# Kernel optimization log

Hardware: AMD Instinct MI355X
Metric: run time of the kernel (lower is better)

The kernel has to match this reference:

```python
import jax, jax.numpy as jnp
import numpy as np

B, HEADS, SCALES, POINTS, HIDDEN = 1, 8, 4, 4, 192
HEAD_DIM = HIDDEN // HEADS
OFFSET_SCALE = 0.35
EPS = 1e-5


def conv1x1(x, W, b=None):
    # x: [B,C,D,H,W], W: [O,C]
    y = jnp.einsum('bcdhw,oc->bodhw', x, W)
    if b is not None:
        y = y + b[None, :, None, None, None]
    return y


def base_grid(D, H, W, dtype):
    z = jnp.linspace(-1.0, 1.0, D, dtype=dtype)
    y = jnp.linspace(-1.0, 1.0, H, dtype=dtype)
    x = jnp.linspace(-1.0, 1.0, W, dtype=dtype)
    zz, yy, xx = jnp.meshgrid(z, y, x, indexing='ij')
    return jnp.stack((xx, yy, zz), axis=-1)  # [D,H,W,3] (x,y,z order)


def trilinear_sample(val, grid):
    # val: [BH,C,Dv,Hv,Wv]; grid: [BH,N,3] normalized (x,y,z), align_corners=False, border padding
    BH, C, Dv, Hv, Wv = val.shape
    unnorm = lambda g, s: jnp.clip(((g + 1.0) * s - 1.0) * 0.5, 0.0, s - 1.0)
    ix = unnorm(grid[..., 0], Wv)
    iy = unnorm(grid[..., 1], Hv)
    iz = unnorm(grid[..., 2], Dv)
    x0f, y0f, z0f = jnp.floor(ix), jnp.floor(iy), jnp.floor(iz)
    wx, wy, wz = ix - x0f, iy - y0f, iz - z0f
    x0 = x0f.astype(jnp.int32); x1 = jnp.minimum(x0 + 1, Wv - 1)
    y0 = y0f.astype(jnp.int32); y1 = jnp.minimum(y0 + 1, Hv - 1)
    z0 = z0f.astype(jnp.int32); z1 = jnp.minimum(z0 + 1, Dv - 1)
    vflat = val.reshape(BH, C, Dv * Hv * Wv)
    gather = jax.vmap(lambda v, i: v[:, i])  # -> [BH,C,N]
    def corner(zi, yi, xi):
        return gather(vflat, (zi * Hv + yi) * Wv + xi)
    w = lambda a: a[:, None, :]  # broadcast weight over channel dim
    out = (corner(z0, y0, x0) * w((1 - wz) * (1 - wy) * (1 - wx))
           + corner(z0, y0, x1) * w((1 - wz) * (1 - wy) * wx)
           + corner(z0, y1, x0) * w((1 - wz) * wy * (1 - wx))
           + corner(z0, y1, x1) * w((1 - wz) * wy * wx)
           + corner(z1, y0, x0) * w(wz * (1 - wy) * (1 - wx))
           + corner(z1, y0, x1) * w(wz * (1 - wy) * wx)
           + corner(z1, y1, x0) * w(wz * wy * (1 - wx))
           + corner(z1, y1, x1) * w(wz * wy * wx))
    return out


def fsad_forward(query_feature, values, Wq, Wvs, Woff, boff, Wwt, bwt, Wout, gamma, beta):
    Bq, _, D, H, W = query_feature.shape
    N = D * H * W
    q = conv1x1(query_feature, Wq)
    off = conv1x1(q, Woff, boff).reshape(Bq, HEADS, SCALES, POINTS, 3, D, H, W)
    off = jnp.tanh(off) * OFFSET_SCALE
    aw = conv1x1(q, Wwt, bwt).reshape(Bq, HEADS, SCALES * POINTS, D, H, W)
    aw = jax.nn.softmax(aw, axis=2).reshape(Bq, HEADS, SCALES, POINTS, D, H, W)
    bg = base_grid(D, H, W, q.dtype)  # [D,H,W,3]
    acc = jnp.zeros((Bq, HEADS, HEAD_DIM, D, H, W), q.dtype)
    for s in range(SCALES):
        feat = values[s]
        val = conv1x1(feat, Wvs[s]).reshape(Bq * HEADS, HEAD_DIM, *feat.shape[2:])
        # off[:,:,s]: [B,Hh,P,3,D,H,W] -> grid [B,Hh,P,D,H,W,3]
        grid = bg[None, None, None] + jnp.moveaxis(off[:, :, s], 3, -1)
        grid = grid.reshape(Bq * HEADS, POINTS * N, 3)
        sampled = trilinear_sample(val, grid).reshape(Bq, HEADS, HEAD_DIM, POINTS, D, H, W)
        acc = acc + jnp.einsum('bhcpdyx,bhpdyx->bhcdyx', sampled, aw[:, :, s])
    out = conv1x1(acc.reshape(Bq, HIDDEN, D, H, W), Wout)
    # InstanceNorm3d(affine=True)
    mu = out.mean(axis=(2, 3, 4), keepdims=True)
    var = out.var(axis=(2, 3, 4), keepdims=True)
    out = (out - mu) * jax.lax.rsqrt(var + EPS)
    return out * gamma[None, :, None, None, None] + beta[None, :, None, None, None]


def setup_inputs() -> dict:
    key = jax.random.key(0)
    ks = jax.random.split(key, 16)
    value_channels = [32, 64, 128, 256]
    sizes = [64, 32, 16, 8]
    inp = {
        'query_feature': jax.random.normal(ks[0], (1, 128, 16, 16, 16), jnp.float32),
        'v0': jax.random.normal(ks[1], (1, 32, 64, 64, 64), jnp.float32),
        'v1': jax.random.normal(ks[2], (1, 64, 32, 32, 32), jnp.float32),
        'v2': jax.random.normal(ks[3], (1, 128, 16, 16, 16), jnp.float32),
        'v3': jax.random.normal(ks[4], (1, 256, 8, 8, 8), jnp.float32),
        'Wq': jax.random.normal(ks[5], (HIDDEN, 128), jnp.float32) * 0.05,
        'Wv0': jax.random.normal(ks[6], (HIDDEN, 32), jnp.float32) * 0.05,
        'Wv1': jax.random.normal(ks[7], (HIDDEN, 64), jnp.float32) * 0.05,
        'Wv2': jax.random.normal(ks[8], (HIDDEN, 128), jnp.float32) * 0.05,
        'Wv3': jax.random.normal(ks[9], (HIDDEN, 256), jnp.float32) * 0.05,
        'Woff': jax.random.normal(ks[10], (HEADS * SCALES * POINTS * 3, HIDDEN), jnp.float32) * 0.05,
        'boff': jnp.zeros((HEADS * SCALES * POINTS * 3,), jnp.float32),
        'Wwt': jax.random.normal(ks[11], (HEADS * SCALES * POINTS, HIDDEN), jnp.float32) * 0.05,
        'bwt': jnp.zeros((HEADS * SCALES * POINTS,), jnp.float32),
        'Wout': jax.random.normal(ks[12], (128, HIDDEN), jnp.float32) * 0.05,
        'gamma': jnp.ones((128,), jnp.float32),
        'beta': jnp.zeros((128,), jnp.float32),
    }
    return inp


def reference(query_feature, v0, v1, v2, v3, Wq, Wv0, Wv1, Wv2, Wv3, Woff, boff, Wwt, bwt, Wout, gamma, beta):
    return fsad_forward(query_feature, [v0, v1, v2, v3], Wq, [Wv0, Wv1, Wv2, Wv3], Woff, boff, Wwt, bwt, Wout, gamma, beta)
```

## Files before the change

### kernel.cpp

```cpp
#include <hip/hip_runtime.h>
#include <hip/hip_fp16.h>
#include <cmath>

#define N_Q 4096
#define HEADS 8
#define HEAD_DIM 24
#define HIDDEN 192

__device__ __forceinline__ float4 ld4(const float* p) { return *(const float4*)p; }

__device__ __forceinline__ void fma8h(float* u, float w, const __half* p) {
    uint4 raw = *(const uint4*)p;
    const __half2* h2 = reinterpret_cast<const __half2*>(&raw);
#pragma unroll
    for (int k = 0; k < 4; k++) {
        float2 f = __half22float2(h2[k]);
        u[2 * k]     = fmaf(w, f.x, u[2 * k]);
        u[2 * k + 1] = fmaf(w, f.y, u[2 * k + 1]);
    }
}

__device__ __forceinline__ void corner24(float* acc, float w, const __half* p) {
    fma8h(acc,      w, p);
    fma8h(acc + 8,  w, p + 8);
    fma8h(acc + 16, w, p + 16);
}


__device__ __forceinline__ void transpose_body(char* smem, const float* __restrict__ src,
                                               __half* __restrict__ dst, int bx, int tid)
{
    float (*lds)[33] = (float(*)[33])smem;
    const int Nv = 262144;
    int pos0 = bx * 256;
    for (int k = tid; k < 256 * 32; k += 256) {
        int c = k >> 8, p = k & 255;
        lds[p][c] = src[(size_t)c * Nv + pos0 + p];
    }
    __syncthreads();
    for (int k = tid; k < 256 * 32; k += 256) {
        int p = k >> 5, c = k & 31;
        dst[(size_t)(pos0 + p) * 32 + c] = __float2half(lds[p][c]);
    }
}

template<int C, int OG>
__device__ __forceinline__ void valconv_body(char* smem, const float* __restrict__ Wv,
                                             const float* __restrict__ v,
                                             __half* __restrict__ valT, int Nv,
                                             int bx, int by, int tid)
{
    float* Wl = (float*)smem;
    __half* outs = (__half*)(smem + OG * C * 4);
    int p0 = bx * 64;
    int og0 = by * OG;
    for (int k = tid; k < OG * C; k += 256) Wl[k] = Wv[(size_t)(og0 + k / C) * C + (k % C)];
    __syncthreads();

    int osub = tid >> 6;
    int lane = tid & 63;
    constexpr int PT = OG / 4;
    float acc[PT];
#pragma unroll
    for (int i = 0; i < PT; i++) acc[i] = 0.f;
#pragma unroll 2
    for (int c = 0; c < C; c++) {
        float vv = v[(size_t)c * Nv + p0 + lane];
#pragma unroll
        for (int i = 0; i < PT; i++)
            acc[i] = fmaf(Wl[(osub * PT + i) * C + c], vv, acc[i]);
    }
#pragma unroll
    for (int i = 0; i < PT; i++)
        outs[lane * OG + osub * PT + i] = __float2half(acc[i]);
    __syncthreads();

    unsigned int* dst = (unsigned int*)valT;
    const unsigned int* src = (const unsigned int*)outs;
    constexpr int UPP = OG / 2;
    for (int k = tid; k < 64 * UPP; k += 256) {
        int p = k / UPP, i = k % UPP;
        int hh = og0 / 24 + i / 12;
        int ii = i % 12;
        dst[((size_t)hh * Nv + p0 + p) * 12 + ii] = src[p * UPP + i];
    }
}

__device__ __forceinline__ void wcomb_body(int bx, int tid,
                                           const float* __restrict__ Woff,
                                           const float* __restrict__ Wwt,
                                           const float* __restrict__ Wq,
                                           const float* __restrict__ boff,
                                           const float* __restrict__ bwt,
                                           float* __restrict__ Wcomb,
                                           float* __restrict__ biasc)
{
    int o = bx * 2 + (tid >> 7);
    int c = tid & 127;
    const float* A = (o < 384) ? (Woff + (size_t)o * 192) : (Wwt + (size_t)(o - 384) * 192);
    float s = 0.f;
#pragma unroll 4
    for (int k = 0; k < 192; k++) s = fmaf(A[k], Wq[k * 128 + c], s);
    Wcomb[(size_t)o * 128 + c] = s;
    if (c == 0) biasc[o] = (o < 384) ? boff[o] : bwt[o - 384];
}

__global__ __launch_bounds__(256)
void prep_kernel(const float* __restrict__ v0, __half* __restrict__ v0T,
                 const float* __restrict__ Wv1, const float* __restrict__ v1, __half* __restrict__ val1T,
                 const float* __restrict__ Wv2, const float* __restrict__ v2, __half* __restrict__ val2T,
                 const float* __restrict__ Wv3, const float* __restrict__ v3, __half* __restrict__ val3T,
                 const float* __restrict__ Woff, const float* __restrict__ Wwt,
                 const float* __restrict__ Wq, const float* __restrict__ boff,
                 const float* __restrict__ bwt, float* __restrict__ Wcomb,
                 float* __restrict__ biasc)
{
    __shared__ __align__(16) char smem[61440];
    int id = blockIdx.x;
    int tid = threadIdx.x;
    if (id < 1024) {
        transpose_body(smem, v0, v0T, id, tid);
    } else if (id < 2048) {
        int i1 = id - 1024;
        valconv_body<64, 96>(smem, Wv1, v1, val1T, 32768, i1 & 511, i1 >> 9, tid);
    } else if (id < 2176) {
        int i2 = id - 2048;
        valconv_body<128, 96>(smem, Wv2, v2, val2T, 4096, i2 & 63, i2 >> 6, tid);
    } else if (id < 2208) {
        int i3 = id - 2176;
        valconv_body<256, 48>(smem, Wv3, v3, val3T, 512, i3 & 7, i3 >> 3, tid);
    } else {
        wcomb_body(id - 2208, tid, Woff, Wwt, Wq, boff, bwt, Wcomb, biasc);
    }
}

__global__ __launch_bounds__(256)
void offaw_kernel(const float* __restrict__ Wcomb, const float* __restrict__ biasc,
                  const float* __restrict__ qf, float* __restrict__ ob)
{
    __shared__ float xs[128 * 64];
    __shared__ float Wl[32 * 128];
    __shared__ float ls[32 * 64];
    int tid = threadIdx.x;
    int n0 = blockIdx.x * 64;
    int og0 = blockIdx.y * 32;
    for (int k = tid; k < 128 * 64; k += 256) xs[k] = qf[(size_t)(k >> 6) * N_Q + n0 + (k & 63)];
    for (int k = tid; k < 32 * 128; k += 256) Wl[k] = Wcomb[(size_t)og0 * 128 + k];
    __syncthreads();

    int wv = tid >> 6, lane = tid & 63;
    float acc[8];
#pragma unroll
    for (int i = 0; i < 8; i++) acc[i] = 0.f;
    for (int c = 0; c < 128; c++) {
        float xv = xs[c * 64 + lane];
#pragma unroll
        for (int i = 0; i < 8; i++)
            acc[i] = fmaf(Wl[(wv * 8 + i) * 128 + c], xv, acc[i]);
    }

    if (og0 < 384) {
#pragma unroll
        for (int i = 0; i < 8; i++) {
            int o = og0 + wv * 8 + i;
            ob[(size_t)o * N_Q + n0 + lane] = tanhf(acc[i] + biasc[o]) * 0.35f;
        }
    } else {
#pragma unroll
        for (int i = 0; i < 8; i++) {
            int o = og0 + wv * 8 + i;
            ls[(wv * 8 + i) * 64 + lane] = acc[i] + biasc[o];
        }
        __syncthreads();
        if (tid < 128) {
            int hl = tid >> 6;
            int n2 = tid & 63;
            float v[16];
            float m = -1e30f;
#pragma unroll
            for (int j = 0; j < 16; j++) { v[j] = ls[(hl * 16 + j) * 64 + n2]; m = fmaxf(m, v[j]); }
            float ssum = 0.f;
#pragma unroll
            for (int j = 0; j < 16; j++) { v[j] = __expf(v[j] - m); ssum += v[j]; }
            float inv = 1.0f / ssum;
            int orow = og0 + hl * 16;
#pragma unroll
            for (int j = 0; j < 16; j++)
                ob[(size_t)(orow + j) * N_Q + n0 + n2] = v[j] * inv;
        }
    }
}

__global__ __launch_bounds__(256)
void sample_kernel(const float* __restrict__ offb, const float* __restrict__ awb,
                   const __half* __restrict__ v0T, const __half* __restrict__ val1T,
                   const __half* __restrict__ val2T, const __half* __restrict__ val3T,
                   const float* __restrict__ Wv0,
                   __half* __restrict__ accb)
{
    int tid = threadIdx.x;
    int id = blockIdx.x;
    int s, h, p, t;
    if (id < 512) {
        s = 0; int r = id & 7; int j = id >> 3;
        t = r + 8 * (j >> 5);
        int rest = j & 31; h = rest >> 2; p = rest & 3;
    } else if (id < 1024) {
        s = 1; int i = id - 512; h = i & 7;
        int j = i >> 3; t = j & 15; p = j >> 4;
    } else {
        int i = id - 1024; s = 2 + (i >> 9);
        int i2 = i & 511; t = i2 & 15; p = (i2 >> 4) & 3; h = i2 >> 6;
    }
    int n = t * 256 + tid;
    int sp = s * 4 + p;

    int wx = n & 15, hy = (n >> 4) & 15, dz = n >> 8;
    const float step = 2.0f / 15.0f;
    float bx = -1.f + wx * step;
    float by = -1.f + hy * step;
    float bz = -1.f + dz * step;

    float acc[HEAD_DIM];
#pragma unroll
    for (int j = 0; j < HEAD_DIM; j++) acc[j] = 0.f;

    int S = 64;
    const __half* srcT = v0T;
    if (s == 1)      { S = 32; srcT = val1T; }
    else if (s == 2) { S = 16; srcT = val2T; }
    else if (s == 3) { S = 8;  srcT = val3T; }
    float fS = (float)S;

    int orow = ((h * 4 + s) * 4 + p) * 3;
    float ox = offb[(orow + 0) * N_Q + n];
    float oy = offb[(orow + 1) * N_Q + n];
    float oz = offb[(orow + 2) * N_Q + n];
    float awv = awb[(h * 16 + s * 4 + p) * N_Q + n];

    float ix = fminf(fmaxf(((bx + ox + 1.f) * fS - 1.f) * 0.5f, 0.f), fS - 1.f);
    float iy = fminf(fmaxf(((by + oy + 1.f) * fS - 1.f) * 0.5f, 0.f), fS - 1.f);
    float iz = fminf(fmaxf(((bz + oz + 1.f) * fS - 1.f) * 0.5f, 0.f), fS - 1.f);

    float x0f = floorf(ix), y0f = floorf(iy), z0f = floorf(iz);
    float fx = ix - x0f, fy = iy - y0f, fz = iz - z0f;
    int x0 = (int)x0f, y0 = (int)y0f, z0 = (int)z0f;
    int x1 = min(x0 + 1, S - 1), y1 = min(y0 + 1, S - 1), z1 = min(z0 + 1, S - 1);

    int r000 = (z0 * S + y0) * S + x0, r001 = (z0 * S + y0) * S + x1;
    int r010 = (z0 * S + y1) * S + x0, r011 = (z0 * S + y1) * S + x1;
    int r100 = (z1 * S + y0) * S + x0, r101 = (z1 * S + y0) * S + x1;
    int r110 = (z1 * S + y1) * S + x0, r111 = (z1 * S + y1) * S + x1;

    float gx1 = fx, gx0 = 1.f - fx;
    float gy1 = fy, gy0 = 1.f - fy;
    float gz1 = fz, gz0 = 1.f - fz;
    float w000 = gz0 * gy0 * gx0 * awv, w001 = gz0 * gy0 * gx1 * awv;
    float w010 = gz0 * gy1 * gx0 * awv, w011 = gz0 * gy1 * gx1 * awv;
    float w100 = gz1 * gy0 * gx0 * awv, w101 = gz1 * gy0 * gx1 * awv;
    float w110 = gz1 * gy1 * gx0 * awv, w111 = gz1 * gy1 * gx1 * awv;

    if (s == 0) {
        const float* Wvh = Wv0 + h * HEAD_DIM * 32;
#pragma unroll
        for (int c8 = 0; c8 < 32; c8 += 8) {
            float u[8] = {0.f, 0.f, 0.f, 0.f, 0.f, 0.f, 0.f, 0.f};
            fma8h(u, w000, srcT + r000 * 32 + c8);
            fma8h(u, w001, srcT + r001 * 32 + c8);
            fma8h(u, w010, srcT + r010 * 32 + c8);
            fma8h(u, w011, srcT + r011 * 32 + c8);
            fma8h(u, w100, srcT + r100 * 32 + c8);
            fma8h(u, w101, srcT + r101 * 32 + c8);
            fma8h(u, w110, srcT + r110 * 32 + c8);
            fma8h(u, w111, srcT + r111 * 32 + c8);
#pragma unroll
            for (int j = 0; j < HEAD_DIM; j++) {
                const float* wp = Wvh + j * 32 + c8;
                float4 wa = ld4(wp), wb = ld4(wp + 4);
                acc[j] = fmaf(wa.x, u[0], fmaf(wa.y, u[1], fmaf(wa.z, u[2], fmaf(wa.w, u[3],
                         fmaf(wb.x, u[4], fmaf(wb.y, u[5], fmaf(wb.z, u[6], fmaf(wb.w, u[7], acc[j]))))))));
            }
        }
    } else {
        int NvS = S * S * S;
        const __half* base = srcT + (size_t)h * NvS * HEAD_DIM;
        corner24(acc, w000, base + (size_t)r000 * HEAD_DIM);
        corner24(acc, w001, base + (size_t)r001 * HEAD_DIM);
        corner24(acc, w010, base + (size_t)r010 * HEAD_DIM);
        corner24(acc, w011, base + (size_t)r011 * HEAD_DIM);
        corner24(acc, w100, base + (size_t)r100 * HEAD_DIM);
        corner24(acc, w101, base + (size_t)r101 * HEAD_DIM);
        corner24(acc, w110, base + (size_t)r110 * HEAD_DIM);
        corner24(acc, w111, base + (size_t)r111 * HEAD_DIM);
    }

    __half* ab = accb + (size_t)sp * HIDDEN * N_Q;
#pragma unroll
    for (int j = 0; j < HEAD_DIM; j++) ab[(h * HEAD_DIM + j) * N_Q + n] = __float2half(acc[j]);
}

__global__ __launch_bounds__(256)
void accsum_kernel(const __half* __restrict__ accb, __half* __restrict__ accsum)
{
    int i = blockIdx.x * 256 + threadIdx.x;
    const int SB8 = HIDDEN * N_Q / 8;
    const uint4* src = (const uint4*)accb;
    float a[8] = {0.f, 0.f, 0.f, 0.f, 0.f, 0.f, 0.f, 0.f};
#pragma unroll
    for (int sp = 0; sp < 16; sp++) {
        uint4 r = src[sp * SB8 + i];
        const __half2* h2 = (const __half2*)&r;
#pragma unroll
        for (int k = 0; k < 4; k++) {
            float2 f = __half22float2(h2[k]);
            a[2 * k] += f.x; a[2 * k + 1] += f.y;
        }
    }
    uint4 o;
    __half2* oh = (__half2*)&o;
#pragma unroll
    for (int k = 0; k < 4; k++)
        oh[k] = __float22half2_rn(make_float2(a[2 * k], a[2 * k + 1]));
    ((uint4*)accsum)[i] = o;
}

__global__ __launch_bounds__(256)
void outconv_kernel(const float* __restrict__ Wout, const __half* __restrict__ accsum,
                    float* __restrict__ out)
{
    __shared__ float xs[HIDDEN * 64];
    __shared__ float Wl[64 * HIDDEN];
    int tid = threadIdx.x;
    int n0 = blockIdx.x * 64;
    int og0 = blockIdx.y * 64;
    for (int k = tid; k < HIDDEN * 8; k += 256) {
        int c = k >> 3, seg = k & 7;
        uint4 r = *(const uint4*)(accsum + (size_t)c * N_Q + n0 + seg * 8);
        const __half2* h2 = (const __half2*)&r;
#pragma unroll
        for (int j = 0; j < 4; j++) {
            float2 f = __half22float2(h2[j]);
            xs[c * 64 + seg * 8 + 2 * j]     = f.x;
            xs[c * 64 + seg * 8 + 2 * j + 1] = f.y;
        }
    }
    for (int k = tid; k < 64 * HIDDEN; k += 256) Wl[k] = Wout[(size_t)og0 * HIDDEN + k];
    __syncthreads();

    int wv = tid >> 6, lane = tid & 63;
    float acc[16];
#pragma unroll
    for (int i = 0; i < 16; i++) acc[i] = 0.f;
    for (int c = 0; c < HIDDEN; c++) {
        float xv = xs[c * 64 + lane];
#pragma unroll
        for (int i = 0; i < 16; i++)
            acc[i] = fmaf(Wl[(wv * 16 + i) * HIDDEN + c], xv, acc[i]);
    }
#pragma unroll
    for (int i = 0; i < 16; i++)
        out[(size_t)(og0 + wv * 16 + i) * N_Q + n0 + lane] = acc[i];
}

__global__ __launch_bounds__(256)
void inorm_kernel(float* __restrict__ out, const float* __restrict__ gamma,
                  const float* __restrict__ beta)
{
    int o = blockIdx.x;
    int tid = threadIdx.x;
    float s = 0.f, s2 = 0.f;
    for (int n = tid; n < N_Q; n += 256) {
        float v = out[o * N_Q + n];
        s += v; s2 += v * v;
    }
    __shared__ float rs[256], rs2[256];
    rs[tid] = s; rs2[tid] = s2;
    __syncthreads();
    for (int k = 128; k > 0; k >>= 1) {
        if (tid < k) { rs[tid] += rs[tid + k]; rs2[tid] += rs2[tid + k]; }
        __syncthreads();
    }
    float mu = rs[0] * (1.0f / N_Q);
    float var = rs2[0] * (1.0f / N_Q) - mu * mu;
    float rstd = rsqrtf(var + 1e-5f);
    float g = gamma[o] * rstd;
    float b = beta[o] - mu * g;
    for (int n = tid; n < N_Q; n += 256) {
        out[o * N_Q + n] = fmaf(out[o * N_Q + n], g, b);
    }
}

extern "C" void kernel_launch(void* const* d_in, const int* in_sizes, int n_in,
                              void* d_out, int out_size, void* d_ws, size_t ws_size,
                              hipStream_t stream)
{
    const float* qf    = (const float*)d_in[0];
    const float* v0    = (const float*)d_in[1];
    const float* v1    = (const float*)d_in[2];
    const float* v2    = (const float*)d_in[3];
    const float* v3    = (const float*)d_in[4];
    const float* Wq    = (const float*)d_in[5];
    const float* Wv0   = (const float*)d_in[6];
    const float* Wv1   = (const float*)d_in[7];
    const float* Wv2   = (const float*)d_in[8];
    const float* Wv3   = (const float*)d_in[9];
    const float* Woff  = (const float*)d_in[10];
    const float* boff  = (const float*)d_in[11];
    const float* Wwt   = (const float*)d_in[12];
    const float* bwt   = (const float*)d_in[13];
    const float* Wout  = (const float*)d_in[14];
    const float* gamma = (const float*)d_in[15];
    const float* beta  = (const float*)d_in[16];
    float* out = (float*)d_out;

    float* ws     = (float*)d_ws;
    float*  Wcomb  = ws;
    float*  biasc  = Wcomb  + 65536;
    float*  offb   = biasc  + 512;
    float*  awb    = offb   + 384 * 4096;
    __half* v0T    = (__half*)(offb + 2097152);
    __half* val1T  = (__half*)((float*)v0T + 4194304);
    __half* val2T  = (__half*)((float*)val1T + 3145728);
    __half* val3T  = (__half*)((float*)val2T + 393216);
    __half* accb   = (__half*)((float*)val3T + 49152);
    __half* accsum = accb + 12582912;

    prep_kernel<<<2464, 256, 0, stream>>>(v0, v0T, Wv1, v1, val1T, Wv2, v2, val2T,
                                          Wv3, v3, val3T, Woff, Wwt, Wq, boff, bwt,
                                          Wcomb, biasc);
    offaw_kernel<<<dim3(64, 16), 256, 0, stream>>>(Wcomb, biasc, qf, offb);
    sample_kernel<<<2048, 256, 0, stream>>>(offb, awb, v0T, val1T, val2T, val3T, Wv0, accb);
    accsum_kernel<<<384, 256, 0, stream>>>(accb, accsum);
    outconv_kernel<<<dim3(64, 2), 256, 0, stream>>>(Wout, accsum, out);
    inorm_kernel<<<128, 256, 0, stream>>>(out, gamma, beta);
}
```

Measured before the change: 279.9 us.

## Restructure value-projection conv to one point per thread with channel-chunked LDS tiles

The value 1x1 conv in the prep kernel is rewritten so each thread owns one spatial point and accumulates 48 output channels (two heads) in registers. Input and weight tiles are streamed through LDS in 16-channel chunks. Results are written as 16-byte vector stores per head instead of being staged and scattered from shared memory. This cuts LDS usage and the block count, which should improve occupancy and store coalescing, at the cost of higher register pressure from the 48 accumulators.

After: 346.7 us. +23.9%, slower.

```diff
diff --git a/kernel.cpp b/kernel.cpp
--- a/kernel.cpp
+++ b/kernel.cpp
@@ -44,45 +44,50 @@
     }
 }
 
-template<int C, int OG>
+template<int C>
 __device__ __forceinline__ void valconv_body(char* smem, const float* __restrict__ Wv,
                                              const float* __restrict__ v,
                                              __half* __restrict__ valT, int Nv,
                                              int bx, int by, int tid)
 {
-    float* Wl = (float*)smem;
-    __half* outs = (__half*)(smem + OG * C * 4);
-    int p0 = bx * 64;
-    int og0 = by * OG;
-    for (int k = tid; k < OG * C; k += 256) Wl[k] = Wv[(size_t)(og0 + k / C) * C + (k % C)];
-    __syncthreads();
-
-    int osub = tid >> 6;
-    int lane = tid & 63;
-    constexpr int PT = OG / 4;
-    float acc[PT];
-#pragma unroll
-    for (int i = 0; i < PT; i++) acc[i] = 0.f;
-#pragma unroll 2
-    for (int c = 0; c < C; c++) {
-        float vv = v[(size_t)c * Nv + p0 + lane];
-#pragma unroll
-        for (int i = 0; i < PT; i++)
-            acc[i] = fmaf(Wl[(osub * PT + i) * C + c], vv, acc[i]);
-    }
-#pragma unroll
-    for (int i = 0; i < PT; i++)
-        outs[lane * OG + osub * PT + i] = __float2half(acc[i]);
-    __syncthreads();
-
-    unsigned int* dst = (unsigned int*)valT;
-    const unsigned int* src = (const unsigned int*)outs;
-    constexpr int UPP = OG / 2;
-    for (int k = tid; k < 64 * UPP; k += 256) {
-        int p = k / UPP, i = k % UPP;
-        int hh = og0 / 24 + i / 12;
-        int ii = i % 12;
-        dst[((size_t)hh * Nv + p0 + p) * 12 + ii] = src[p * UPP + i];
+    float (*vbuf)[256] = (float(*)[256])smem;
+    float (*wbuf)[16]  = (float(*)[16])(smem + 16 * 256 * 4);
+    int p0 = bx * 256;
+    int og0 = by * 48;
+    float acc[48];
+#pragma unroll
+    for (int i = 0; i < 48; i++) acc[i] = 0.f;
+
+    for (int c0 = 0; c0 < C; c0 += 16) {
+        for (int k = tid; k < 16 * 256; k += 256) {
+            int cc = k >> 8, pp = k & 255;
+            vbuf[cc][pp] = v[(size_t)(c0 + cc) * Nv + p0 + pp];
+        }
+        for (int k = tid; k < 48 * 16; k += 256) {
+            int o = k >> 4, cc = k & 15;
+            wbuf[o][cc] = Wv[(size_t)(og0 + o) * C + c0 + cc];
+        }
+        __syncthreads();
+#pragma unroll 4
+        for (int cc = 0; cc < 16; cc++) {
+            float vv = vbuf[cc][tid];
+#pragma unroll
+            for (int o = 0; o < 48; o++)
+                acc[o] = fmaf(wbuf[o][cc], vv, acc[o]);
+        }
+        __syncthreads();
+    }
+
+    int p = p0 + tid;
+#pragma unroll
+    for (int q = 0; q < 2; q++) {
+        int h = og0 / 24 + q;
+        __half tmp[24];
+#pragma unroll
+        for (int j = 0; j < 24; j++) tmp[j] = __float2half(acc[q * 24 + j]);
+        uint4* dst = (uint4*)(valT + ((size_t)h * Nv + p) * 24);
+        const uint4* s4 = (const uint4*)tmp;
+        dst[0] = s4[0]; dst[1] = s4[1]; dst[2] = s4[2];
     }
 }
 
@@ -115,22 +120,22 @@
                  const float* __restrict__ bwt, float* __restrict__ Wcomb,
                  float* __restrict__ biasc)
 {
-    __shared__ __align__(16) char smem[61440];
+    __shared__ __align__(16) char smem[33792];
     int id = blockIdx.x;
     int tid = threadIdx.x;
     if (id < 1024) {
         transpose_body(smem, v0, v0T, id, tid);
-    } else if (id < 2048) {
+    } else if (id < 1536) {
         int i1 = id - 1024;
-        valconv_body<64, 96>(smem, Wv1, v1, val1T, 32768, i1 & 511, i1 >> 9, tid);
-    } else if (id < 2176) {
-        int i2 = id - 2048;
-        valconv_body<128, 96>(smem, Wv2, v2, val2T, 4096, i2 & 63, i2 >> 6, tid);
-    } else if (id < 2208) {
-        int i3 = id - 2176;
-        valconv_body<256, 48>(smem, Wv3, v3, val3T, 512, i3 & 7, i3 >> 3, tid);
+        valconv_body<64>(smem, Wv1, v1, val1T, 32768, i1 & 127, i1 >> 7, tid);
+    } else if (id < 1600) {
+        int i2 = id - 1536;
+        valconv_body<128>(smem, Wv2, v2, val2T, 4096, i2 & 15, i2 >> 4, tid);
+    } else if (id < 1608) {
+        int i3 = id - 1600;
+        valconv_body<256>(smem, Wv3, v3, val3T, 512, i3 & 1, i3 >> 1, tid);
     } else {
-        wcomb_body(id - 2208, tid, Woff, Wwt, Wq, boff, bwt, Wcomb, biasc);
+        wcomb_body(id - 1608, tid, Woff, Wwt, Wq, boff, bwt, Wcomb, biasc);
     }
 }
 
@@ -425,7 +430,7 @@
     __half* accb   = (__half*)((float*)val3T + 49152);
     __half* accsum = accb + 12582912;
 
-    prep_kernel<<<2464, 256, 0, stream>>>(v0, v0T, Wv1, v1, val1T, Wv2, v2, val2T,
+    prep_kernel<<<1864, 256, 0, stream>>>(v0, v0T, Wv1, v1, val1T, Wv2, v2, val2T,
                                           Wv3, v3, val3T, Woff, Wwt, Wq, boff, bwt,
                                           Wcomb, biasc);
     offaw_kernel<<<dim3(64, 16), 256, 0, stream>>>(Wcomb, biasc, qf, offb);
```

## Split value projection into per-head blocks with direct half stores

Applied to the files above, without the earlier changes.

The value-projection part of the prep kernel is changed from blocks covering 96 or 48 output channels to one block per head, which is 24 channels. Each thread now computes 6 channels, reads four input channels per step, and loads the weights from LDS as float4. Results are written straight to global memory as packed halves, so the LDS staging buffer and second sync are gone. This cuts shared memory, which should raise occupancy, and adds more blocks. The cost is that the input activations are re-read once per head, and each thread does 12-byte stores with a 48-byte stride, which coalesce less well.

Measured after the change: 262.2 us. -6.3%, faster.

```diff
diff --git a/kernel.cpp b/kernel.cpp
--- a/kernel.cpp
+++ b/kernel.cpp
@@ -44,46 +44,43 @@
     }
 }
 
-template<int C, int OG>
-__device__ __forceinline__ void valconv_body(char* smem, const float* __restrict__ Wv,
-                                             const float* __restrict__ v,
-                                             __half* __restrict__ valT, int Nv,
-                                             int bx, int by, int tid)
+template<int C>
+__device__ __forceinline__ void valconv24_body(char* smem, const float* __restrict__ Wv,
+                                               const float* __restrict__ v,
+                                               __half* __restrict__ valT, int Nv,
+                                               int bx, int h, int tid)
 {
     float* Wl = (float*)smem;
-    __half* outs = (__half*)(smem + OG * C * 4);
     int p0 = bx * 64;
-    int og0 = by * OG;
-    for (int k = tid; k < OG * C; k += 256) Wl[k] = Wv[(size_t)(og0 + k / C) * C + (k % C)];
+    for (int k = tid; k < 24 * C; k += 256)
+        Wl[k] = Wv[(size_t)(h * 24 + k / C) * C + (k % C)];
     __syncthreads();
 
     int osub = tid >> 6;
     int lane = tid & 63;
-    constexpr int PT = OG / 4;
-    float acc[PT];
-#pragma unroll
-    for (int i = 0; i < PT; i++) acc[i] = 0.f;
-#pragma unroll 2
-    for (int c = 0; c < C; c++) {
-        float vv = v[(size_t)c * Nv + p0 + lane];
-#pragma unroll
-        for (int i = 0; i < PT; i++)
-            acc[i] = fmaf(Wl[(osub * PT + i) * C + c], vv, acc[i]);
-    }
-#pragma unroll
-    for (int i = 0; i < PT; i++)
-        outs[lane * OG + osub * PT + i] = __float2half(acc[i]);
-    __syncthreads();
-
-    unsigned int* dst = (unsigned int*)valT;
-    const unsigned int* src = (const unsigned int*)outs;
-    constexpr int UPP = OG / 2;
-    for (int k = tid; k < 64 * UPP; k += 256) {
-        int p = k / UPP, i = k % UPP;
-        int hh = og0 / 24 + i / 12;
-        int ii = i % 12;
-        dst[((size_t)hh * Nv + p0 + p) * 12 + ii] = src[p * UPP + i];
-    }
+    int p = p0 + lane;
+    float acc[6];
+#pragma unroll
+    for (int i = 0; i < 6; i++) acc[i] = 0.f;
+
+    for (int c = 0; c < C; c += 4) {
+        float va = v[(size_t)c * Nv + p];
+        float vb = v[(size_t)(c + 1) * Nv + p];
+        float vc = v[(size_t)(c + 2) * Nv + p];
+        float vd = v[(size_t)(c + 3) * Nv + p];
+#pragma unroll
+        for (int i = 0; i < 6; i++) {
+            float4 w4 = *(const float4*)&Wl[(osub * 6 + i) * C + c];
+            acc[i] = fmaf(w4.x, va, fmaf(w4.y, vb, fmaf(w4.z, vc, fmaf(w4.w, vd, acc[i]))));
+        }
+    }
+
+    __half tmp[6];
+#pragma unroll
+    for (int i = 0; i < 6; i++) tmp[i] = __float2half(acc[i]);
+    unsigned int* dst = (unsigned int*)(valT + ((size_t)h * Nv + p) * 24 + osub * 6);
+    const unsigned int* s4 = (const unsigned int*)tmp;
+    dst[0] = s4[0]; dst[1] = s4[1]; dst[2] = s4[2];
 }
 
 __device__ __forceinline__ void wcomb_body(int bx, int tid,
@@ -115,22 +112,22 @@
                  const float* __restrict__ bwt, float* __restrict__ Wcomb,
                  float* __restrict__ biasc)
 {
-    __shared__ __align__(16) char smem[61440];
+    __shared__ __align__(16) char smem[33792];
     int id = blockIdx.x;
     int tid = threadIdx.x;
     if (id < 1024) {
         transpose_body(smem, v0, v0T, id, tid);
-    } else if (id < 2048) {
+    } else if (id < 5120) {
         int i1 = id - 1024;
-        valconv_body<64, 96>(smem, Wv1, v1, val1T, 32768, i1 & 511, i1 >> 9, tid);
-    } else if (id < 2176) {
-        int i2 = id - 2048;
-        valconv_body<128, 96>(smem, Wv2, v2, val2T, 4096, i2 & 63, i2 >> 6, tid);
-    } else if (id < 2208) {
-        int i3 = id - 2176;
-        valconv_body<256, 48>(smem, Wv3, v3, val3T, 512, i3 & 7, i3 >> 3, tid);
+        valconv24_body<64>(smem, Wv1, v1, val1T, 32768, i1 & 511, i1 >> 9, tid);
+    } else if (id < 5632) {
+        int i2 = id - 5120;
+        valconv24_body<128>(smem, Wv2, v2, val2T, 4096, i2 & 63, i2 >> 6, tid);
+    } else if (id < 5696) {
+        int i3 = id - 5632;
+        valconv24_body<256>(smem, Wv3, v3, val3T, 512, i3 & 7, i3 >> 3, tid);
     } else {
-        wcomb_body(id - 2208, tid, Woff, Wwt, Wq, boff, bwt, Wcomb, biasc);
+        wcomb_body(id - 5696, tid, Woff, Wwt, Wq, boff, bwt, Wcomb, biasc);
     }
 }
 
@@ -425,7 +422,7 @@
     __half* accb   = (__half*)((float*)val3T + 49152);
     __half* accsum = accb + 12582912;
 
-    prep_kernel<<<2464, 256, 0, stream>>>(v0, v0T, Wv1, v1, val1T, Wv2, v2, val2T,
+    prep_kernel<<<5952, 256, 0, stream>>>(v0, v0T, Wv1, v1, val1T, Wv2, v2, val2T,
                                           Wv3, v3, val3T, Woff, Wwt, Wq, boff, bwt,
                                           Wcomb, biasc);
     offaw_kernel<<<dim3(64, 16), 256, 0, stream>>>(Wcomb, biasc, qf, offb);
```
